# Kernel tuning notes

Measured on AMD Instinct MI355X. Metric: run time of the kernel, lower is better.

The kernel has to match this reference:

```python
import jax, jax.numpy as jnp
import numpy as np

DIM = 768
NUM_HEADS = 12
KERNEL = 3
DILATIONS = (1, 2, 3)


def setup_inputs() -> dict:
    key = jax.random.key(0)
    k1, k2, k3, k4 = jax.random.split(key, 4)
    B, N, C = 4, 4096, DIM
    return {
        "x": jax.random.normal(k1, (B, N, C), jnp.float32),
        "w_qkv": jax.random.normal(k2, (3 * C, C), jnp.float32) * 0.02,
        "w_proj": jax.random.normal(k3, (C, C), jnp.float32) * 0.02,
        "b_proj": jax.random.normal(k4, (C,), jnp.float32) * 0.02,
    }


def _dilate_attention(q, k, v, dilation, head_dim, kernel):
    # q,k,v: [B, d, N] where d = C / num_dilation
    B, d, N = q.shape
    h = d // head_dim
    scale = head_dim ** -0.5
    qh = q.reshape(B, h, head_dim, N)
    kh = k.reshape(B, h, head_dim, N)
    vh = v.reshape(B, h, head_dim, N)
    pad = dilation * (kernel - 1) // 2

    def windows(t):
        # gather the `kernel` dilated neighbors along N with zero padding
        tp = jnp.pad(t, ((0, 0), (0, 0), (0, 0), (pad, pad)))
        return jnp.stack([tp[..., j * dilation: j * dilation + N] for j in range(kernel)], axis=3)  # [B,h,hd,kernel,N]

    k_win = windows(kh)
    v_win = windows(vh)
    scores = jnp.einsum('bhdn,bhdkn->bhnk', qh, k_win) * scale  # [B,h,N,kernel]
    # Torch nn.Unfold on the [B,d,N,1] 'image' yields kernel*kernel columns;
    # only the center width-column is real, the rest are zero padding -> score 0.
    kk = kernel * kernel
    center = (kernel - 1) // 2
    scores_full = jnp.zeros(scores.shape[:3] + (kk,), scores.dtype).at[..., center::kernel].set(scores)
    probs = jax.nn.softmax(scores_full, axis=-1)  # zero-key columns dilute the softmax, faithfully
    probs_real = probs[..., center::kernel]  # [B,h,N,kernel]; zero-key columns multiply zero values
    out = jnp.einsum('bhnk,bhdkn->bhnd', probs_real, v_win)  # [B,h,N,hd]
    return out.transpose(0, 2, 1, 3).reshape(B, N, d)


def reference(x, w_qkv, w_proj, b_proj):
    B, N, C = x.shape
    nd = len(DILATIONS)
    head_dim = C // NUM_HEADS
    # [B,N,3C] -> [B,N,3,nd,C/nd] -> [nd,3,B,C/nd,N]
    qkv = (x @ w_qkv.T).reshape(B, N, 3, nd, C // nd).transpose(3, 2, 0, 4, 1)
    outs = [_dilate_attention(qkv[i, 0], qkv[i, 1], qkv[i, 2], DILATIONS[i], head_dim, KERNEL)
            for i in range(nd)]
    xo = jnp.stack(outs, axis=2).reshape(B, N, C)  # [B,N,nd,d] -> [B,N,C]
    xo = xo @ w_proj.T + b_proj
    # matches torch return (x, x2=None, v, k, q); x2 omitted (is_decoder=False)
    return (xo, qkv[:, 2], qkv[:, 1], qkv[:, 0])
```

## Files before the change

### kernel.cpp

```cpp
#include <hip/hip_runtime.h>

typedef __attribute__((ext_vector_type(8))) short bf16x8;
typedef __attribute__((ext_vector_type(4))) float f32x4;

#define SZQKV 12582912

__device__ __forceinline__ unsigned short f2bf(float f) {
    unsigned int u = __float_as_uint(f);
    unsigned int r = (u + 0x7FFFu + ((u >> 16) & 1u)) >> 16;
    return (unsigned short)r;
}

#define GLDS16(g, l) __builtin_amdgcn_global_load_lds( \
    (const __attribute__((address_space(1))) unsigned int*)(g), \
    (__attribute__((address_space(3))) unsigned int*)(l), 16, 0, 0)

__global__ void cast_all(const float* __restrict__ x,
                         const float* __restrict__ wqkv,
                         const float* __restrict__ wproj,
                         unsigned short* __restrict__ dst) {
    const int T1 = 12582912;
    const int T2 = T1 + 1769472;
    const int T3 = T2 + 589824;
    int stride = gridDim.x * blockDim.x * 4;
    for (int base = (blockIdx.x * blockDim.x + threadIdx.x) * 4; base < T3; base += stride) {
        const float* src; int off;
        if (base < T1)      { src = x;     off = base; }
        else if (base < T2) { src = wqkv;  off = base - T1; }
        else                { src = wproj; off = base - T2; }
        float4 v = *(const float4*)(src + off);
        ushort4 o;
        o.x = f2bf(v.x); o.y = f2bf(v.y); o.z = f2bf(v.z); o.w = f2bf(v.w);
        *(ushort4*)(dst + base) = o;
    }
}

template <int MODE>
__global__ __launch_bounds__(512, 2) void gemm8(const unsigned short* __restrict__ A,
                                                const unsigned short* __restrict__ Bw,
                                                const float* __restrict__ bias,
                                                float* __restrict__ dout,
                                                int nby) {
    __shared__ unsigned char lds8[131072];
    const int t = threadIdx.x;
    const int lane = t & 63;
    const int w = t >> 6;
    const int wm = w >> 2;
    const int wn = w & 3;

    const int cpx = gridDim.x >> 3;
    const int orig = blockIdx.x;
    const int wgid = (orig & 7) * cpx + (orig >> 3);
    const int bx = wgid / nby, by = wgid - bx * nby;
    const int m0 = bx * 256;
    const int n0 = by * 256;

    const unsigned char* Ab = (const unsigned char*)A;
    const unsigned char* Bb = (const unsigned char*)Bw;

    const int trow = t >> 3;
    const int jx = ((t & 7) ^ (trow & 7)) << 4;
    const size_t aBase = (size_t)(m0 + trow) * 1536 + jx;
    const size_t bBase = (size_t)(n0 + trow) * 1536 + jx;
    const int ldst = t * 16;

    const int rA = wm * 128 + (lane & 15);
    const int rB = wn * 64 + (lane & 15);
    const int xt0 = (((lane >> 4)) ^ (lane & 7)) << 4;
    const int xt1 = ((4 + (lane >> 4)) ^ (lane & 7)) << 4;

    f32x4 acc[8][4] = {};

#define STAGE(kt, bsel) do { \
    unsigned char* db_ = lds8 + (bsel) * 65536; \
    const size_t ko_ = (size_t)(kt) * 128; \
    GLDS16(Ab + aBase + ko_,          db_ + ldst); \
    GLDS16(Ab + aBase + ko_ + 98304,  db_ + ldst + 8192); \
    GLDS16(Ab + aBase + ko_ + 196608, db_ + ldst + 16384); \
    GLDS16(Ab + aBase + ko_ + 294912, db_ + ldst + 24576); \
    GLDS16(Bb + bBase + ko_,          db_ + 32768 + ldst); \
    GLDS16(Bb + bBase + ko_ + 98304,  db_ + 32768 + ldst + 8192); \
    GLDS16(Bb + bBase + ko_ + 196608, db_ + 32768 + ldst + 16384); \
    GLDS16(Bb + bBase + ko_ + 294912, db_ + 32768 + ldst + 24576); \
} while (0)

#define LDA4(base_, xt_) do { \
    _Pragma("unroll") \
    for (int mi = 0; mi < 4; ++mi) \
        av[mi] = *(const bf16x8*)(bufA + (rA + (base_) + mi * 16) * 128 + (xt_)); \
} while (0)

#define LDB4(xt_) do { \
    _Pragma("unroll") \
    for (int ni = 0; ni < 4; ++ni) \
        bv[ni] = *(const bf16x8*)(bufB + (rB + ni * 16) * 128 + (xt_)); \
} while (0)

#define MM(rbase_) do { \
    __builtin_amdgcn_s_setprio(1); \
    _Pragma("unroll") \
    for (int mi = 0; mi < 4; ++mi) \
    _Pragma("unroll") \
    for (int ni = 0; ni < 4; ++ni) \
        acc[(rbase_) + mi][ni] = __builtin_amdgcn_mfma_f32_16x16x32_bf16(av[mi], bv[ni], acc[(rbase_) + mi][ni], 0, 0, 0); \
    __builtin_amdgcn_s_setprio(0); \
} while (0)

    STAGE(0, 0);
    for (int kt = 0; kt < 12; ++kt) {
        if (kt < 11) {
            STAGE(kt + 1, (kt + 1) & 1);
            asm volatile("s_waitcnt vmcnt(8)" ::: "memory");
        } else {
            asm volatile("s_waitcnt vmcnt(0)" ::: "memory");
        }
        __builtin_amdgcn_s_barrier();
        asm volatile("" ::: "memory");
        const unsigned char* bufA = lds8 + (kt & 1) * 65536;
        const unsigned char* bufB = bufA + 32768;
        bf16x8 av[4], bv[4];
        LDA4(0, xt0); LDB4(xt0); MM(0);
        LDA4(64, xt0); MM(4);
        LDA4(0, xt1); LDB4(xt1); MM(0);
        LDA4(64, xt1); MM(4);
        asm volatile("s_waitcnt lgkmcnt(0)" ::: "memory");
        __builtin_amdgcn_s_barrier();
        asm volatile("" ::: "memory");
    }
#undef STAGE
#undef LDA4
#undef LDB4
#undef MM

    const int crow = (lane >> 4) * 4;
    const int ccol = lane & 15;
    if (MODE == 0) {
        const int b = m0 >> 12;
        const int n_base = m0 & 4095;
#pragma unroll
        for (int mi = 0; mi < 8; ++mi) {
            int n = n_base + wm * 128 + mi * 16 + crow;
#pragma unroll
            for (int ni = 0; ni < 4; ++ni) {
                int o = n0 + wn * 64 + ni * 16 + ccol;
                int sel = o / 768;
                int rem = o - sel * 768;
                float* dst = dout + (size_t)(3 - sel) * SZQKV
                           + ((size_t)((rem >> 8) * 4 + b) * 256 + (rem & 255)) * 4096 + n;
                *(f32x4*)dst = acc[mi][ni];
            }
        }
    } else {
#pragma unroll
        for (int mi = 0; mi < 8; ++mi) {
            int m = m0 + wm * 128 + mi * 16 + crow;
#pragma unroll
            for (int ni = 0; ni < 4; ++ni) {
                int o = n0 + wn * 64 + ni * 16 + ccol;
                float bb = bias[o];
#pragma unroll
                for (int r = 0; r < 4; ++r)
                    dout[(size_t)(m + r) * 768 + o] = acc[mi][ni][r] + bb;
            }
        }
    }
}

__global__ __launch_bounds__(256) void attn_kernel(const float* __restrict__ qkv,
                                                   unsigned short* __restrict__ attnbf) {
    const int chunk = blockIdx.x;
    const int dil_i = blockIdx.y;
    const int b     = blockIdx.z;
    const int dil   = dil_i + 1;
    const int t  = threadIdx.x;
    const int h  = t >> 6;
    const int nl = t & 63;
    const int n  = chunk * 64 + nl;

    const size_t gb = (size_t)(dil_i * 4 + b) * 256 * 4096;
    const float* Q = qkv + (size_t)3 * SZQKV + gb;
    const float* K = qkv + (size_t)2 * SZQKV + gb;
    const float* V = qkv + (size_t)1 * SZQKV + gb;

    const int nm = n - dil, np = n + dil;
    const bool vm = (nm >= 0), vp = (np < 4096);
    const int nmc = vm ? nm : 0, npc = vp ? np : 4095;

    float s0 = 0.f, s1 = 0.f, s2 = 0.f;
    {
        const float* qrow = Q + (size_t)h * 64 * 4096;
        const float* krow = K + (size_t)h * 64 * 4096;
        for (int d = 0; d < 64; ++d) {
            float q = qrow[n];
            s0 += q * krow[nmc];
            s1 += q * krow[n];
            s2 += q * krow[npc];
            qrow += 4096; krow += 4096;
        }
    }
    s0 = vm ? s0 * 0.125f : 0.f;
    s1 *= 0.125f;
    s2 = vp ? s2 * 0.125f : 0.f;
    float mx = fmaxf(0.f, fmaxf(s0, fmaxf(s1, s2)));
    float e0 = __expf(s0 - mx), e1 = __expf(s1 - mx), e2 = __expf(s2 - mx);
    float den = e0 + e1 + e2 + 6.f * __expf(-mx);
    float inv = 1.f / den;
    float p0 = vm ? e0 * inv : 0.f;
    float p1 = e1 * inv;
    float p2 = vp ? e2 * inv : 0.f;

    __shared__ unsigned short lout[256][65];
    {
        const float* vrow = V + (size_t)h * 64 * 4096;
        for (int d = 0; d < 64; ++d) {
            float o = p0 * vrow[nmc] + p1 * vrow[n] + p2 * vrow[npc];
            lout[h * 64 + d][nl] = f2bf(o);
            vrow += 4096;
        }
    }
    __syncthreads();

#pragma unroll
    for (int i = 0; i < 8; ++i) {
        int linear = i * 256 + t;
        int nn   = linear >> 5;
        int cblk = linear & 31;
        union { unsigned short u[8]; f32x4 v; } tt;
#pragma unroll
        for (int j = 0; j < 8; ++j) tt.u[j] = lout[cblk * 8 + j][nn];
        unsigned short* dst = attnbf + (size_t)(b * 4096 + chunk * 64 + nn) * 768
                            + dil_i * 256 + cblk * 8;
        *(f32x4*)dst = tt.v;
    }
}

extern "C" void kernel_launch(void* const* d_in, const int* in_sizes, int n_in,
                              void* d_out, int out_size, void* d_ws, size_t ws_size,
                              hipStream_t stream) {
    const float* x     = (const float*)d_in[0];
    const float* wqkv  = (const float*)d_in[1];
    const float* wproj = (const float*)d_in[2];
    const float* bproj = (const float*)d_in[3];
    float* out = (float*)d_out;

    unsigned short* xbf     = (unsigned short*)d_ws;
    unsigned short* wqkvbf  = xbf + 12582912;
    unsigned short* wprojbf = wqkvbf + 1769472;
    unsigned short* attnbf  = wprojbf + 589824;

    cast_all<<<2048, 256, 0, stream>>>(x, wqkv, wproj, xbf);

    gemm8<0><<<dim3(576), 512, 0, stream>>>(xbf, wqkvbf, nullptr, out, 9);

    attn_kernel<<<dim3(64, 3, 4), 256, 0, stream>>>(out, attnbf);

    gemm8<1><<<dim3(192), 512, 0, stream>>>(attnbf, wprojbf, bproj, out, 3);
}
```

Measured before the change: 178.8 us.

## Fuse x fp32-to-bf16 cast into QKV GEMM and stage epilogues through LDS

The separate cast of x to bf16 is dropped. The QKV GEMM now loads fp32 x tiles into registers, packs them to bf16 (round-half-up via a perm instruction) and writes them into swizzled LDS, double-buffered against the B-tile async loads. This removes a full 50MB read and 25MB write pass over x. Both GEMM epilogues now transpose the accumulators through LDS so global stores are fully coalesced 16-byte rows; the projection epilogue also loads its bias as a vector. The risks are extra register pressure, an extra global-load round trip in the main loop, and a slightly different bf16 rounding mode for x.

```diff
diff --git a/kernel.cpp b/kernel.cpp
--- a/kernel.cpp
+++ b/kernel.cpp
@@ -11,23 +11,26 @@
     return (unsigned short)r;
 }
 
+__device__ __forceinline__ unsigned int pack2bf(float lo, float hi) {
+    unsigned int ul = __float_as_uint(lo) + 0x8000u;
+    unsigned int uh = __float_as_uint(hi) + 0x8000u;
+    return __builtin_amdgcn_perm(uh, ul, 0x07060302u);
+}
+
 #define GLDS16(g, l) __builtin_amdgcn_global_load_lds( \
     (const __attribute__((address_space(1))) unsigned int*)(g), \
     (__attribute__((address_space(3))) unsigned int*)(l), 16, 0, 0)
 
-__global__ void cast_all(const float* __restrict__ x,
-                         const float* __restrict__ wqkv,
-                         const float* __restrict__ wproj,
-                         unsigned short* __restrict__ dst) {
-    const int T1 = 12582912;
-    const int T2 = T1 + 1769472;
-    const int T3 = T2 + 589824;
+__global__ void cast_w(const float* __restrict__ wqkv,
+                       const float* __restrict__ wproj,
+                       unsigned short* __restrict__ dst) {
+    const int T1 = 1769472;
+    const int T2 = T1 + 589824;
     int stride = gridDim.x * blockDim.x * 4;
-    for (int base = (blockIdx.x * blockDim.x + threadIdx.x) * 4; base < T3; base += stride) {
+    for (int base = (blockIdx.x * blockDim.x + threadIdx.x) * 4; base < T2; base += stride) {
         const float* src; int off;
-        if (base < T1)      { src = x;     off = base; }
-        else if (base < T2) { src = wqkv;  off = base - T1; }
-        else                { src = wproj; off = base - T2; }
+        if (base < T1) { src = wqkv; off = base; }
+        else           { src = wproj; off = base - T1; }
         float4 v = *(const float4*)(src + off);
         ushort4 o;
         o.x = f2bf(v.x); o.y = f2bf(v.y); o.z = f2bf(v.z); o.w = f2bf(v.w);
@@ -35,25 +38,186 @@
     }
 }
 
-template <int MODE>
-__global__ __launch_bounds__(512, 2) void gemm8(const unsigned short* __restrict__ A,
-                                                const unsigned short* __restrict__ Bw,
-                                                const float* __restrict__ bias,
-                                                float* __restrict__ dout,
-                                                int nby) {
+#define LDA4(base_, xt_) do { \
+    _Pragma("unroll") \
+    for (int mi = 0; mi < 4; ++mi) \
+        av[mi] = *(const bf16x8*)(bufA + (rA + (base_) + mi * 16) * 128 + (xt_)); \
+} while (0)
+
+#define LDB4(xt_) do { \
+    _Pragma("unroll") \
+    for (int ni = 0; ni < 4; ++ni) \
+        bv[ni] = *(const bf16x8*)(bufB + (rB + ni * 16) * 128 + (xt_)); \
+} while (0)
+
+#define MM(rbase_) do { \
+    __builtin_amdgcn_s_setprio(1); \
+    _Pragma("unroll") \
+    for (int mi = 0; mi < 4; ++mi) \
+    _Pragma("unroll") \
+    for (int ni = 0; ni < 4; ++ni) \
+        acc[(rbase_) + mi][ni] = __builtin_amdgcn_mfma_f32_16x16x32_bf16(av[mi], bv[ni], acc[(rbase_) + mi][ni], 0, 0, 0); \
+    __builtin_amdgcn_s_setprio(0); \
+} while (0)
+
+__global__ __launch_bounds__(512, 2) void gemm_qkv(const float* __restrict__ X,
+                                                   const unsigned short* __restrict__ Bw,
+                                                   float* __restrict__ dout) {
     __shared__ unsigned char lds8[131072];
     const int t = threadIdx.x;
     const int lane = t & 63;
     const int w = t >> 6;
-    const int wm = w >> 2;
-    const int wn = w & 3;
+    const int wm = w >> 2, wn = w & 3;
 
     const int cpx = gridDim.x >> 3;
     const int orig = blockIdx.x;
     const int wgid = (orig & 7) * cpx + (orig >> 3);
-    const int bx = wgid / nby, by = wgid - bx * nby;
-    const int m0 = bx * 256;
-    const int n0 = by * 256;
+    const int bx = wgid / 9, by = wgid - bx * 9;
+    const int m0 = bx * 256, n0 = by * 256;
+
+    const unsigned char* Xb = (const unsigned char*)X;
+    const unsigned char* Bb = (const unsigned char*)Bw;
+
+    const int arow = t >> 3;
+    const int aj = t & 7;
+    const size_t aSrc = (size_t)(m0 + arow) * 3072 + aj * 32;
+    const int aDst = arow * 128 + ((aj ^ (arow & 7)) << 4);
+
+    const int jx = ((t & 7) ^ (arow & 7)) << 4;
+    const size_t bSrc = (size_t)(n0 + arow) * 1536 + jx;
+    const int ldst = t * 16;
+
+    const int rA = wm * 128 + (lane & 15);
+    const int rB = wn * 64 + (lane & 15);
+    const int xt0 = (((lane >> 4)) ^ (lane & 7)) << 4;
+    const int xt1 = ((4 + (lane >> 4)) ^ (lane & 7)) << 4;
+
+    f32x4 acc[8][4] = {};
+    f32x4 ar[8];
+
+#define ALOAD(kt) do { \
+    const unsigned char* s_ = Xb + aSrc + (size_t)(kt) * 256; \
+    _Pragma("unroll") \
+    for (int g = 0; g < 4; ++g) { \
+        ar[2*g]   = *(const f32x4*)(s_ + (size_t)g * 196608); \
+        ar[2*g+1] = *(const f32x4*)(s_ + (size_t)g * 196608 + 16); \
+    } \
+} while (0)
+
+#define BSTAGE(kt, bsel) do { \
+    unsigned char* db_ = lds8 + (bsel) * 65536 + 32768; \
+    const size_t ko_ = (size_t)(kt) * 128; \
+    GLDS16(Bb + bSrc + ko_,          db_ + ldst); \
+    GLDS16(Bb + bSrc + ko_ + 98304,  db_ + ldst + 8192); \
+    GLDS16(Bb + bSrc + ko_ + 196608, db_ + ldst + 16384); \
+    GLDS16(Bb + bSrc + ko_ + 294912, db_ + ldst + 24576); \
+} while (0)
+
+#define AWRITE(bsel) do { \
+    unsigned char* da_ = lds8 + (bsel) * 65536; \
+    _Pragma("unroll") \
+    for (int g = 0; g < 4; ++g) { \
+        uint4 pv; \
+        pv.x = pack2bf(ar[2*g][0],   ar[2*g][1]); \
+        pv.y = pack2bf(ar[2*g][2],   ar[2*g][3]); \
+        pv.z = pack2bf(ar[2*g+1][0], ar[2*g+1][1]); \
+        pv.w = pack2bf(ar[2*g+1][2], ar[2*g+1][3]); \
+        *(uint4*)(da_ + aDst + g * 8192) = pv; \
+    } \
+} while (0)
+
+    ALOAD(0);
+    asm volatile("" ::: "memory");
+    BSTAGE(0, 0);
+    asm volatile("s_waitcnt vmcnt(4)" ::: "memory");
+    AWRITE(0);
+    asm volatile("s_waitcnt lgkmcnt(0)" ::: "memory");
+
+    for (int kt = 0; kt < 12; ++kt) {
+        if (kt < 11) {
+            ALOAD(kt + 1);
+            asm volatile("" ::: "memory");
+            BSTAGE(kt + 1, (kt + 1) & 1);
+            asm volatile("s_waitcnt vmcnt(12)" ::: "memory");
+        } else {
+            asm volatile("s_waitcnt vmcnt(0)" ::: "memory");
+        }
+        __builtin_amdgcn_s_barrier();
+        asm volatile("" ::: "memory");
+        const unsigned char* bufA = lds8 + (kt & 1) * 65536;
+        const unsigned char* bufB = bufA + 32768;
+        bf16x8 av[4], bv[4];
+        LDA4(0, xt0); LDB4(xt0); MM(0);
+        LDA4(64, xt0); MM(4);
+        LDA4(0, xt1); LDB4(xt1); MM(0);
+        LDA4(64, xt1); MM(4);
+        if (kt < 11) {
+            asm volatile("s_waitcnt vmcnt(4)" ::: "memory");
+            AWRITE((kt + 1) & 1);
+        }
+        asm volatile("s_waitcnt lgkmcnt(0)" ::: "memory");
+        __builtin_amdgcn_s_barrier();
+        asm volatile("" ::: "memory");
+    }
+#undef ALOAD
+#undef BSTAGE
+#undef AWRITE
+
+    float* ldsf = (float*)lds8;
+    const int bidx = m0 >> 12;
+    const int n_base = m0 & 4095;
+    const int ccol = lane & 15;
+    const int hi4 = (lane >> 4) * 4;
+#pragma unroll
+    for (int h = 0; h < 2; ++h) {
+        if ((wn >> 1) == h) {
+            const int o2b = (wn & 1) * 64;
+#pragma unroll
+            for (int mi = 0; mi < 8; ++mi)
+#pragma unroll
+                for (int ni = 0; ni < 4; ++ni) {
+                    int o2 = o2b + ni * 16 + ccol;
+                    int nl = wm * 128 + mi * 16 + hi4;
+                    *(f32x4*)&ldsf[o2 * 256 + (nl ^ ((o2 & 7) << 2))] = acc[mi][ni];
+                }
+        }
+        asm volatile("s_waitcnt lgkmcnt(0)" ::: "memory");
+        __builtin_amdgcn_s_barrier();
+        asm volatile("" ::: "memory");
+#pragma unroll 4
+        for (int it = 0; it < 16; ++it) {
+            int row = w * 16 + it;
+            int o = n0 + h * 128 + row;
+            int sel = o / 768;
+            int rem = o - sel * 768;
+            f32x4 v = *(const f32x4*)&ldsf[row * 256 + ((lane * 4) ^ ((row & 7) << 2))];
+            float* dst = dout + (size_t)(3 - sel) * SZQKV
+                       + ((size_t)((rem >> 8) * 4 + bidx) * 256 + (rem & 255)) * 4096
+                       + n_base + lane * 4;
+            *(f32x4*)dst = v;
+        }
+        if (h == 0) {
+            __builtin_amdgcn_s_barrier();
+            asm volatile("" ::: "memory");
+        }
+    }
+}
+
+__global__ __launch_bounds__(512, 2) void gemm_proj(const unsigned short* __restrict__ A,
+                                                    const unsigned short* __restrict__ Bw,
+                                                    const float* __restrict__ bias,
+                                                    float* __restrict__ dout) {
+    __shared__ unsigned char lds8[131072];
+    const int t = threadIdx.x;
+    const int lane = t & 63;
+    const int w = t >> 6;
+    const int wm = w >> 2, wn = w & 3;
+
+    const int cpx = gridDim.x >> 3;
+    const int orig = blockIdx.x;
+    const int wgid = (orig & 7) * cpx + (orig >> 3);
+    const int bx = wgid / 3, by = wgid - bx * 3;
+    const int m0 = bx * 256, n0 = by * 256;
 
     const unsigned char* Ab = (const unsigned char*)A;
     const unsigned char* Bb = (const unsigned char*)Bw;
@@ -84,28 +248,6 @@
     GLDS16(Bb + bBase + ko_ + 294912, db_ + 32768 + ldst + 24576); \
 } while (0)
 
-#define LDA4(base_, xt_) do { \
-    _Pragma("unroll") \
-    for (int mi = 0; mi < 4; ++mi) \
-        av[mi] = *(const bf16x8*)(bufA + (rA + (base_) + mi * 16) * 128 + (xt_)); \
-} while (0)
-
-#define LDB4(xt_) do { \
-    _Pragma("unroll") \
-    for (int ni = 0; ni < 4; ++ni) \
-        bv[ni] = *(const bf16x8*)(bufB + (rB + ni * 16) * 128 + (xt_)); \
-} while (0)
-
-#define MM(rbase_) do { \
-    __builtin_amdgcn_s_setprio(1); \
-    _Pragma("unroll") \
-    for (int mi = 0; mi < 4; ++mi) \
-    _Pragma("unroll") \
-    for (int ni = 0; ni < 4; ++ni) \
-        acc[(rbase_) + mi][ni] = __builtin_amdgcn_mfma_f32_16x16x32_bf16(av[mi], bv[ni], acc[(rbase_) + mi][ni], 0, 0, 0); \
-    __builtin_amdgcn_s_setprio(0); \
-} while (0)
-
     STAGE(0, 0);
     for (int kt = 0; kt < 12; ++kt) {
         if (kt < 11) {
@@ -128,40 +270,39 @@
         asm volatile("" ::: "memory");
     }
 #undef STAGE
-#undef LDA4
-#undef LDB4
-#undef MM
-
-    const int crow = (lane >> 4) * 4;
+
+    float* ldsf = (float*)lds8;
     const int ccol = lane & 15;
-    if (MODE == 0) {
-        const int b = m0 >> 12;
-        const int n_base = m0 & 4095;
-#pragma unroll
-        for (int mi = 0; mi < 8; ++mi) {
-            int n = n_base + wm * 128 + mi * 16 + crow;
-#pragma unroll
-            for (int ni = 0; ni < 4; ++ni) {
-                int o = n0 + wn * 64 + ni * 16 + ccol;
-                int sel = o / 768;
-                int rem = o - sel * 768;
-                float* dst = dout + (size_t)(3 - sel) * SZQKV
-                           + ((size_t)((rem >> 8) * 4 + b) * 256 + (rem & 255)) * 4096 + n;
-                *(f32x4*)dst = acc[mi][ni];
-            }
-        }
-    } else {
-#pragma unroll
-        for (int mi = 0; mi < 8; ++mi) {
-            int m = m0 + wm * 128 + mi * 16 + crow;
-#pragma unroll
-            for (int ni = 0; ni < 4; ++ni) {
-                int o = n0 + wn * 64 + ni * 16 + ccol;
-                float bb = bias[o];
-#pragma unroll
-                for (int r = 0; r < 4; ++r)
-                    dout[(size_t)(m + r) * 768 + o] = acc[mi][ni][r] + bb;
-            }
+    const int hi4 = (lane >> 4) * 4;
+#pragma unroll
+    for (int h = 0; h < 2; ++h) {
+        if (wm == h) {
+#pragma unroll
+            for (int mi = 0; mi < 8; ++mi)
+#pragma unroll
+                for (int ni = 0; ni < 4; ++ni) {
+                    int o = wn * 64 + ni * 16 + ccol;
+                    int m2b = mi * 16 + hi4;
+#pragma unroll
+                    for (int r = 0; r < 4; ++r)
+                        ldsf[(m2b + r) * 256 + (o ^ (((m2b + r) & 7) << 2))] = acc[mi][ni][r];
+                }
+        }
+        asm volatile("s_waitcnt lgkmcnt(0)" ::: "memory");
+        __builtin_amdgcn_s_barrier();
+        asm volatile("" ::: "memory");
+        f32x4 bv4 = *(const f32x4*)(bias + n0 + lane * 4);
+#pragma unroll 4
+        for (int it = 0; it < 16; ++it) {
+            int m2 = w * 16 + it;
+            f32x4 v = *(const f32x4*)&ldsf[m2 * 256 + ((lane * 4) ^ ((m2 & 7) << 2))];
+            v = v + bv4;
+            float* dst = dout + (size_t)(m0 + h * 128 + m2) * 768 + n0 + lane * 4;
+            *(f32x4*)dst = v;
+        }
+        if (h == 0) {
+            __builtin_amdgcn_s_barrier();
+            asm volatile("" ::: "memory");
         }
     }
 }
@@ -243,16 +384,15 @@
     const float* bproj = (const float*)d_in[3];
     float* out = (float*)d_out;
 
-    unsigned short* xbf     = (unsigned short*)d_ws;
-    unsigned short* wqkvbf  = xbf + 12582912;
+    unsigned short* wqkvbf  = (unsigned short*)d_ws;
     unsigned short* wprojbf = wqkvbf + 1769472;
     unsigned short* attnbf  = wprojbf + 589824;
 
-    cast_all<<<2048, 256, 0, stream>>>(x, wqkv, wproj, xbf);
-
-    gemm8<0><<<dim3(576), 512, 0, stream>>>(xbf, wqkvbf, nullptr, out, 9);
+    cast_w<<<1152, 256, 0, stream>>>(wqkv, wproj, wqkvbf);
+
+    gemm_qkv<<<dim3(576), 512, 0, stream>>>(x, wqkvbf, out);
 
     attn_kernel<<<dim3(64, 3, 4), 256, 0, stream>>>(out, attnbf);
 
-    gemm8<1><<<dim3(192), 512, 0, stream>>>(attnbf, wprojbf, bproj, out, 3);
-}
+    gemm_proj<<<dim3(192), 512, 0, stream>>>(attnbf, wprojbf, bproj, out);
+}
```

Measured after the change: 195.9 us. 1.1x slower.

## Split K-tile staging into half-tiles interleaved with MFMA and stage epilogue through LDS

Applied to the files above, without the earlier changes.

The GEMM mainloop now stages each 128-byte K tile as two 64-byte sub-tiles, with a new swizzle. Global-to-LDS loads for the next tile are issued between MFMA groups, so memory traffic overlaps compute instead of being issued all at once before a barrier. The epilogue writes accumulators to LDS and then stores fully coalesced float4 rows to global memory, for both the transposed QKV output and the bias-added projection output. This adds more barriers per iteration and extra LDS round trips in the epilogue, and it leaves a dead STG macro behind.

```diff
diff --git a/kernel.cpp b/kernel.cpp
--- a/kernel.cpp
+++ b/kernel.cpp
@@ -45,55 +45,55 @@
     const int t = threadIdx.x;
     const int lane = t & 63;
     const int w = t >> 6;
-    const int wm = w >> 2;
-    const int wn = w & 3;
+    const int wm = w >> 2, wn = w & 3;
 
     const int cpx = gridDim.x >> 3;
     const int orig = blockIdx.x;
     const int wgid = (orig & 7) * cpx + (orig >> 3);
     const int bx = wgid / nby, by = wgid - bx * nby;
-    const int m0 = bx * 256;
-    const int n0 = by * 256;
+    const int m0 = bx * 256, n0 = by * 256;
 
     const unsigned char* Ab = (const unsigned char*)A;
     const unsigned char* Bb = (const unsigned char*)Bw;
 
-    const int trow = t >> 3;
-    const int jx = ((t & 7) ^ (trow & 7)) << 4;
-    const size_t aBase = (size_t)(m0 + trow) * 1536 + jx;
-    const size_t bBase = (size_t)(n0 + trow) * 1536 + jx;
+    const int srow = t >> 2;
+    const int sc = ((t & 3) ^ (srow & 3)) << 4;
+    const size_t aSrc = (size_t)(m0 + srow) * 1536 + sc;
+    const size_t bSrc = (size_t)(n0 + srow) * 1536 + sc;
     const int ldst = t * 16;
 
     const int rA = wm * 128 + (lane & 15);
     const int rB = wn * 64 + (lane & 15);
-    const int xt0 = (((lane >> 4)) ^ (lane & 7)) << 4;
-    const int xt1 = ((4 + (lane >> 4)) ^ (lane & 7)) << 4;
+    const int xt = (((lane >> 4)) ^ (lane & 3)) << 4;
 
     f32x4 acc[8][4] = {};
 
-#define STAGE(kt, bsel) do { \
-    unsigned char* db_ = lds8 + (bsel) * 65536; \
-    const size_t ko_ = (size_t)(kt) * 128; \
-    GLDS16(Ab + aBase + ko_,          db_ + ldst); \
-    GLDS16(Ab + aBase + ko_ + 98304,  db_ + ldst + 8192); \
-    GLDS16(Ab + aBase + ko_ + 196608, db_ + ldst + 16384); \
-    GLDS16(Ab + aBase + ko_ + 294912, db_ + ldst + 24576); \
-    GLDS16(Bb + bBase + ko_,          db_ + 32768 + ldst); \
-    GLDS16(Bb + bBase + ko_ + 98304,  db_ + 32768 + ldst + 8192); \
-    GLDS16(Bb + bBase + ko_ + 196608, db_ + 32768 + ldst + 16384); \
-    GLDS16(Bb + bBase + ko_ + 294912, db_ + 32768 + ldst + 24576); \
-} while (0)
-
-#define LDA4(base_, xt_) do { \
+#define STG(reg_, srcb_, kt_, ks_) do { \
+    const size_t so_ = (srcb_) + (size_t)(kt_) * 128 + (ks_) * 64; \
+    GLDS16((ks_ ? Ab : Ab) + 0, (unsigned char*)0); \
+} while (0)
+#undef STG
+#define STGA(regptr_, kt_, ks_) do { \
+    const size_t so_ = aSrc + (size_t)(kt_) * 128 + (ks_) * 64; \
+    GLDS16(Ab + so_,          (regptr_) + ldst); \
+    GLDS16(Ab + so_ + 196608, (regptr_) + 8192 + ldst); \
+} while (0)
+#define STGB(regptr_, kt_, ks_) do { \
+    const size_t so_ = bSrc + (size_t)(kt_) * 128 + (ks_) * 64; \
+    GLDS16(Bb + so_,          (regptr_) + 8192 * 0 + ldst); \
+    GLDS16(Bb + so_ + 196608, (regptr_) + 8192 + ldst); \
+} while (0)
+
+#define LDA4(cb_, ks_, mb_) do { \
     _Pragma("unroll") \
     for (int mi = 0; mi < 4; ++mi) \
-        av[mi] = *(const bf16x8*)(bufA + (rA + (base_) + mi * 16) * 128 + (xt_)); \
-} while (0)
-
-#define LDB4(xt_) do { \
+        av[mi] = *(const bf16x8*)((cb_) + (ks_) * 16384 + (rA + (mb_) + mi * 16) * 64 + xt); \
+} while (0)
+
+#define LDB4(cb_, ks_) do { \
     _Pragma("unroll") \
     for (int ni = 0; ni < 4; ++ni) \
-        bv[ni] = *(const bf16x8*)(bufB + (rB + ni * 16) * 128 + (xt_)); \
+        bv[ni] = *(const bf16x8*)((cb_) + 32768 + (ks_) * 16384 + (rB + ni * 16) * 64 + xt); \
 } while (0)
 
 #define MM(rbase_) do { \
@@ -106,62 +106,113 @@
     __builtin_amdgcn_s_setprio(0); \
 } while (0)
 
-    STAGE(0, 0);
+#define BAR() do { __builtin_amdgcn_s_barrier(); asm volatile("" ::: "memory"); } while (0)
+
+    {
+        unsigned char* b0 = lds8;
+        unsigned char* b1 = lds8 + 65536;
+        STGA(b0,          0, 0);
+        STGA(b0 + 16384,  0, 1);
+        STGB(b0 + 32768,  0, 0);
+        STGB(b0 + 49152,  0, 1);
+        STGA(b1,          1, 0);
+        asm volatile("s_waitcnt vmcnt(2)" ::: "memory");
+        BAR();
+    }
+
     for (int kt = 0; kt < 12; ++kt) {
-        if (kt < 11) {
-            STAGE(kt + 1, (kt + 1) & 1);
-            asm volatile("s_waitcnt vmcnt(8)" ::: "memory");
-        } else {
-            asm volatile("s_waitcnt vmcnt(0)" ::: "memory");
-        }
-        __builtin_amdgcn_s_barrier();
-        asm volatile("" ::: "memory");
-        const unsigned char* bufA = lds8 + (kt & 1) * 65536;
-        const unsigned char* bufB = bufA + 32768;
+        unsigned char* cb = lds8 + (kt & 1) * 65536;
+        unsigned char* nb = lds8 + ((kt + 1) & 1) * 65536;
         bf16x8 av[4], bv[4];
-        LDA4(0, xt0); LDB4(xt0); MM(0);
-        LDA4(64, xt0); MM(4);
-        LDA4(0, xt1); LDB4(xt1); MM(0);
-        LDA4(64, xt1); MM(4);
-        asm volatile("s_waitcnt lgkmcnt(0)" ::: "memory");
-        __builtin_amdgcn_s_barrier();
-        asm volatile("" ::: "memory");
-    }
-#undef STAGE
+        LDA4(cb, 0, 0); LDB4(cb, 0);
+        if (kt < 11) STGA(nb + 16384, kt + 1, 1);
+        MM(0);
+        BAR();
+        LDA4(cb, 0, 64);
+        if (kt < 11) STGB(nb + 32768, kt + 1, 0);
+        MM(4);
+        BAR();
+        LDA4(cb, 1, 0); LDB4(cb, 1);
+        if (kt < 11) STGB(nb + 49152, kt + 1, 1);
+        MM(0);
+        BAR();
+        LDA4(cb, 1, 64);
+        if (kt < 10) STGA(cb, kt + 2, 0);
+        MM(4);
+        if (kt < 10)      asm volatile("s_waitcnt vmcnt(2)" ::: "memory");
+        else if (kt == 10) asm volatile("s_waitcnt vmcnt(0)" ::: "memory");
+        BAR();
+    }
+#undef STGA
+#undef STGB
 #undef LDA4
 #undef LDB4
 #undef MM
 
-    const int crow = (lane >> 4) * 4;
     const int ccol = lane & 15;
+    const int hi4 = (lane >> 4) * 4;
+    float* ldsf = (float*)lds8;
     if (MODE == 0) {
-        const int b = m0 >> 12;
+        const int bidx = m0 >> 12;
         const int n_base = m0 & 4095;
 #pragma unroll
-        for (int mi = 0; mi < 8; ++mi) {
-            int n = n_base + wm * 128 + mi * 16 + crow;
-#pragma unroll
-            for (int ni = 0; ni < 4; ++ni) {
-                int o = n0 + wn * 64 + ni * 16 + ccol;
+        for (int h = 0; h < 2; ++h) {
+            if ((wn >> 1) == h) {
+                const int o2b = (wn & 1) * 64;
+#pragma unroll
+                for (int mi = 0; mi < 8; ++mi)
+#pragma unroll
+                    for (int ni = 0; ni < 4; ++ni) {
+                        int o2 = o2b + ni * 16 + ccol;
+                        int nl = wm * 128 + mi * 16 + hi4;
+                        *(f32x4*)&ldsf[o2 * 256 + (nl ^ ((o2 & 7) << 2))] = acc[mi][ni];
+                    }
+            }
+            asm volatile("s_waitcnt lgkmcnt(0)" ::: "memory");
+            __builtin_amdgcn_s_barrier();
+            asm volatile("" ::: "memory");
+#pragma unroll 4
+            for (int it = 0; it < 16; ++it) {
+                int row = w * 16 + it;
+                int o = n0 + h * 128 + row;
                 int sel = o / 768;
                 int rem = o - sel * 768;
+                f32x4 v = *(const f32x4*)&ldsf[row * 256 + ((lane * 4) ^ ((row & 7) << 2))];
                 float* dst = dout + (size_t)(3 - sel) * SZQKV
-                           + ((size_t)((rem >> 8) * 4 + b) * 256 + (rem & 255)) * 4096 + n;
-                *(f32x4*)dst = acc[mi][ni];
+                           + ((size_t)((rem >> 8) * 4 + bidx) * 256 + (rem & 255)) * 4096
+                           + n_base + lane * 4;
+                *(f32x4*)dst = v;
             }
+            if (h == 0) { __builtin_amdgcn_s_barrier(); asm volatile("" ::: "memory"); }
         }
     } else {
 #pragma unroll
-        for (int mi = 0; mi < 8; ++mi) {
-            int m = m0 + wm * 128 + mi * 16 + crow;
-#pragma unroll
-            for (int ni = 0; ni < 4; ++ni) {
-                int o = n0 + wn * 64 + ni * 16 + ccol;
-                float bb = bias[o];
-#pragma unroll
-                for (int r = 0; r < 4; ++r)
-                    dout[(size_t)(m + r) * 768 + o] = acc[mi][ni][r] + bb;
+        for (int h = 0; h < 2; ++h) {
+            if (wm == h) {
+#pragma unroll
+                for (int mi = 0; mi < 8; ++mi)
+#pragma unroll
+                    for (int ni = 0; ni < 4; ++ni) {
+                        int o = wn * 64 + ni * 16 + ccol;
+                        int m2b = mi * 16 + hi4;
+#pragma unroll
+                        for (int r = 0; r < 4; ++r)
+                            ldsf[(m2b + r) * 256 + (o ^ (((m2b + r) & 7) << 2))] = acc[mi][ni][r];
+                    }
             }
+            asm volatile("s_waitcnt lgkmcnt(0)" ::: "memory");
+            __builtin_amdgcn_s_barrier();
+            asm volatile("" ::: "memory");
+            f32x4 bv4 = *(const f32x4*)(bias + n0 + lane * 4);
+#pragma unroll 4
+            for (int it = 0; it < 16; ++it) {
+                int m2 = w * 16 + it;
+                f32x4 v = *(const f32x4*)&ldsf[m2 * 256 + ((lane * 4) ^ ((m2 & 7) << 2))];
+                v = v + bv4;
+                float* dst = dout + (size_t)(m0 + h * 128 + m2) * 768 + n0 + lane * 4;
+                *(f32x4*)dst = v;
+            }
+            if (h == 0) { __builtin_amdgcn_s_barrier(); asm volatile("" ::: "memory"); }
         }
     }
 }
```

Result: no change. 176.7 us (-1.2%).

## Shrink GEMM tiles to 256x128 with 4 waves and stage epilogue through LDS

Applied to the files above, without the earlier changes.

Replaces the 512-thread 256x256 GEMM with a 256-thread kernel using 256x128 tiles and a K-step of 32, with a smaller LDS footprint so three blocks can share a CU. The grid doubles, which targets wave quantization and occupancy on the many-CU device. The epilogue is also rewritten to transpose accumulators through swizzled LDS so global stores are coalesced, for both the transposed QKV scatter and the bias-added projection output. In exchange it performs more K iterations with barriers and gets less operand reuse per tile.

```diff
diff --git a/kernel.cpp b/kernel.cpp
--- a/kernel.cpp
+++ b/kernel.cpp
@@ -36,64 +36,59 @@
 }
 
 template <int MODE>
-__global__ __launch_bounds__(512, 2) void gemm8(const unsigned short* __restrict__ A,
+__global__ __launch_bounds__(256, 3) void gemm4(const unsigned short* __restrict__ A,
                                                 const unsigned short* __restrict__ Bw,
                                                 const float* __restrict__ bias,
                                                 float* __restrict__ dout,
                                                 int nby) {
-    __shared__ unsigned char lds8[131072];
+    __shared__ unsigned char lds8[49152];
     const int t = threadIdx.x;
     const int lane = t & 63;
     const int w = t >> 6;
-    const int wm = w >> 2;
-    const int wn = w & 3;
+    const int wm = w >> 1, wn = w & 1;
 
     const int cpx = gridDim.x >> 3;
     const int orig = blockIdx.x;
     const int wgid = (orig & 7) * cpx + (orig >> 3);
     const int bx = wgid / nby, by = wgid - bx * nby;
-    const int m0 = bx * 256;
-    const int n0 = by * 256;
+    const int m0 = bx * 256, n0 = by * 128;
 
     const unsigned char* Ab = (const unsigned char*)A;
     const unsigned char* Bb = (const unsigned char*)Bw;
 
-    const int trow = t >> 3;
-    const int jx = ((t & 7) ^ (trow & 7)) << 4;
-    const size_t aBase = (size_t)(m0 + trow) * 1536 + jx;
-    const size_t bBase = (size_t)(n0 + trow) * 1536 + jx;
+    const int srow = t >> 2;
+    const int sc = ((t & 3) ^ (srow & 3)) << 4;
+    const size_t aBase = (size_t)(m0 + srow) * 1536 + sc;
+    const size_t bBase = (size_t)(n0 + srow) * 1536 + sc;
     const int ldst = t * 16;
 
     const int rA = wm * 128 + (lane & 15);
     const int rB = wn * 64 + (lane & 15);
-    const int xt0 = (((lane >> 4)) ^ (lane & 7)) << 4;
-    const int xt1 = ((4 + (lane >> 4)) ^ (lane & 7)) << 4;
+    const int xt = (((lane >> 4)) ^ (lane & 3)) << 4;
 
     f32x4 acc[8][4] = {};
 
 #define STAGE(kt, bsel) do { \
-    unsigned char* db_ = lds8 + (bsel) * 65536; \
-    const size_t ko_ = (size_t)(kt) * 128; \
+    unsigned char* db_ = lds8 + (bsel) * 24576; \
+    const size_t ko_ = (size_t)(kt) * 64; \
     GLDS16(Ab + aBase + ko_,          db_ + ldst); \
-    GLDS16(Ab + aBase + ko_ + 98304,  db_ + ldst + 8192); \
-    GLDS16(Ab + aBase + ko_ + 196608, db_ + ldst + 16384); \
-    GLDS16(Ab + aBase + ko_ + 294912, db_ + ldst + 24576); \
-    GLDS16(Bb + bBase + ko_,          db_ + 32768 + ldst); \
-    GLDS16(Bb + bBase + ko_ + 98304,  db_ + 32768 + ldst + 8192); \
-    GLDS16(Bb + bBase + ko_ + 196608, db_ + 32768 + ldst + 16384); \
-    GLDS16(Bb + bBase + ko_ + 294912, db_ + 32768 + ldst + 24576); \
-} while (0)
-
-#define LDA4(base_, xt_) do { \
+    GLDS16(Ab + aBase + ko_ + 98304,  db_ + ldst + 4096); \
+    GLDS16(Ab + aBase + ko_ + 196608, db_ + ldst + 8192); \
+    GLDS16(Ab + aBase + ko_ + 294912, db_ + ldst + 12288); \
+    GLDS16(Bb + bBase + ko_,          db_ + 16384 + ldst); \
+    GLDS16(Bb + bBase + ko_ + 98304,  db_ + 16384 + ldst + 4096); \
+} while (0)
+
+#define LDA4(mb_) do { \
     _Pragma("unroll") \
     for (int mi = 0; mi < 4; ++mi) \
-        av[mi] = *(const bf16x8*)(bufA + (rA + (base_) + mi * 16) * 128 + (xt_)); \
-} while (0)
-
-#define LDB4(xt_) do { \
+        av[mi] = *(const bf16x8*)(bufA + (rA + (mb_) + mi * 16) * 64 + xt); \
+} while (0)
+
+#define LDB4() do { \
     _Pragma("unroll") \
     for (int ni = 0; ni < 4; ++ni) \
-        bv[ni] = *(const bf16x8*)(bufB + (rB + ni * 16) * 128 + (xt_)); \
+        bv[ni] = *(const bf16x8*)(bufB + (rB + ni * 16) * 64 + xt); \
 } while (0)
 
 #define MM(rbase_) do { \
@@ -107,22 +102,20 @@
 } while (0)
 
     STAGE(0, 0);
-    for (int kt = 0; kt < 12; ++kt) {
-        if (kt < 11) {
+    for (int kt = 0; kt < 24; ++kt) {
+        if (kt < 23) {
             STAGE(kt + 1, (kt + 1) & 1);
-            asm volatile("s_waitcnt vmcnt(8)" ::: "memory");
+            asm volatile("s_waitcnt vmcnt(6)" ::: "memory");
         } else {
             asm volatile("s_waitcnt vmcnt(0)" ::: "memory");
         }
         __builtin_amdgcn_s_barrier();
         asm volatile("" ::: "memory");
-        const unsigned char* bufA = lds8 + (kt & 1) * 65536;
-        const unsigned char* bufB = bufA + 32768;
+        const unsigned char* bufA = lds8 + (kt & 1) * 24576;
+        const unsigned char* bufB = bufA + 16384;
         bf16x8 av[4], bv[4];
-        LDA4(0, xt0); LDB4(xt0); MM(0);
-        LDA4(64, xt0); MM(4);
-        LDA4(0, xt1); LDB4(xt1); MM(0);
-        LDA4(64, xt1); MM(4);
+        LDA4(0); LDB4(); MM(0);
+        LDA4(64); MM(4);
         asm volatile("s_waitcnt lgkmcnt(0)" ::: "memory");
         __builtin_amdgcn_s_barrier();
         asm volatile("" ::: "memory");
@@ -132,35 +125,80 @@
 #undef LDB4
 #undef MM
 
-    const int crow = (lane >> 4) * 4;
     const int ccol = lane & 15;
+    const int hi4 = (lane >> 4) * 4;
+    float* ldsf = (float*)lds8;
     if (MODE == 0) {
-        const int b = m0 >> 12;
+        const int bidx = m0 >> 12;
         const int n_base = m0 & 4095;
 #pragma unroll
-        for (int mi = 0; mi < 8; ++mi) {
-            int n = n_base + wm * 128 + mi * 16 + crow;
-#pragma unroll
-            for (int ni = 0; ni < 4; ++ni) {
-                int o = n0 + wn * 64 + ni * 16 + ccol;
+        for (int s = 0; s < 4; ++s) {
+            if (wn == (s >> 1)) {
+#pragma unroll
+                for (int mi = 0; mi < 8; ++mi)
+#pragma unroll
+                    for (int j = 0; j < 2; ++j) {
+                        int ni = (s & 1) * 2 + j;
+                        int o2 = j * 16 + ccol;
+                        int nl = wm * 128 + mi * 16 + hi4;
+                        *(f32x4*)&ldsf[o2 * 256 + (nl ^ ((o2 & 7) << 2))] = acc[mi][ni];
+                    }
+            }
+            asm volatile("s_waitcnt lgkmcnt(0)" ::: "memory");
+            __builtin_amdgcn_s_barrier();
+            asm volatile("" ::: "memory");
+#pragma unroll
+            for (int it = 0; it < 8; ++it) {
+                int row = w * 8 + it;
+                int o = n0 + s * 32 + row;
                 int sel = o / 768;
                 int rem = o - sel * 768;
+                f32x4 v = *(const f32x4*)&ldsf[row * 256 + ((lane * 4) ^ ((row & 7) << 2))];
                 float* dst = dout + (size_t)(3 - sel) * SZQKV
-                           + ((size_t)((rem >> 8) * 4 + b) * 256 + (rem & 255)) * 4096 + n;
-                *(f32x4*)dst = acc[mi][ni];
+                           + ((size_t)((rem >> 8) * 4 + bidx) * 256 + (rem & 255)) * 4096
+                           + n_base + lane * 4;
+                *(f32x4*)dst = v;
+            }
+            if (s < 3) {
+                asm volatile("s_waitcnt lgkmcnt(0)" ::: "memory");
+                __builtin_amdgcn_s_barrier();
+                asm volatile("" ::: "memory");
             }
         }
     } else {
 #pragma unroll
-        for (int mi = 0; mi < 8; ++mi) {
-            int m = m0 + wm * 128 + mi * 16 + crow;
-#pragma unroll
-            for (int ni = 0; ni < 4; ++ni) {
-                int o = n0 + wn * 64 + ni * 16 + ccol;
-                float bb = bias[o];
-#pragma unroll
-                for (int r = 0; r < 4; ++r)
-                    dout[(size_t)(m + r) * 768 + o] = acc[mi][ni][r] + bb;
+        for (int s = 0; s < 4; ++s) {
+            if (wm == (s >> 1)) {
+#pragma unroll
+                for (int mj = 0; mj < 4; ++mj) {
+                    int mi = (s & 1) * 4 + mj;
+#pragma unroll
+                    for (int ni = 0; ni < 4; ++ni) {
+                        int o = wn * 64 + ni * 16 + ccol;
+                        int m2b = mj * 16 + hi4;
+#pragma unroll
+                        for (int r = 0; r < 4; ++r)
+                            ldsf[(m2b + r) * 128 + (o ^ (((m2b + r) & 7) << 2))] = acc[mi][ni][r];
+                    }
+                }
+            }
+            asm volatile("s_waitcnt lgkmcnt(0)" ::: "memory");
+            __builtin_amdgcn_s_barrier();
+            asm volatile("" ::: "memory");
+            float b0 = bias[n0 + lane * 2];
+            float b1 = bias[n0 + lane * 2 + 1];
+#pragma unroll
+            for (int it = 0; it < 16; ++it) {
+                int m2 = w * 16 + it;
+                float2 v = *(const float2*)&ldsf[m2 * 128 + ((lane * 2) ^ ((m2 & 7) << 2))];
+                v.x += b0; v.y += b1;
+                float* dst = dout + (size_t)(m0 + s * 64 + m2) * 768 + n0 + lane * 2;
+                *(float2*)dst = v;
+            }
+            if (s < 3) {
+                asm volatile("s_waitcnt lgkmcnt(0)" ::: "memory");
+                __builtin_amdgcn_s_barrier();
+                asm volatile("" ::: "memory");
             }
         }
     }
@@ -250,9 +288,9 @@
 
     cast_all<<<2048, 256, 0, stream>>>(x, wqkv, wproj, xbf);
 
-    gemm8<0><<<dim3(576), 512, 0, stream>>>(xbf, wqkvbf, nullptr, out, 9);
+    gemm4<0><<<dim3(1152), 256, 0, stream>>>(xbf, wqkvbf, nullptr, out, 18);
 
     attn_kernel<<<dim3(64, 3, 4), 256, 0, stream>>>(out, attnbf);
 
-    gemm8<1><<<dim3(192), 512, 0, stream>>>(attnbf, wprojbf, bproj, out, 3);
-}
+    gemm4<1><<<dim3(384), 256, 0, stream>>>(attnbf, wprojbf, bproj, out, 6);
+}
```

After: 193.6 us. 1.08x slower.
